# Kernel optimization log

Hardware: AMD Instinct MI355X
Metric: run time of the kernel (lower is better)

The kernel has to match this reference:

```python
import jax, jax.numpy as jnp
import numpy as np

EPS_NUMER = 1e-8   # numerator init in original code
EPS_D2 = 1e-12     # guard sqrt(0) on the (unused) diagonal


def setup_inputs() -> dict:
    key = jax.random.key(0)
    k0, k1, k2, k3 = jax.random.split(key, 4)
    B, T, C, H, W, D, NC = 128, 128, 3, 32, 32, 1024, 10
    data_t = jax.random.normal(k0, (B, T, 1, C, H, W), jnp.float32)
    responses_t = jax.random.normal(k1, (B, T, NC), jnp.float32)
    teaching_signal_t = jax.random.uniform(k2, (B, T, NC), jnp.float32)
    # feature extractor = single linear layer; scaled so distances are moderate
    W_fe = jax.random.normal(k3, (C * H * W, D), jnp.float32) / np.float32(np.sqrt(C * H * W))
    b_fe = jnp.zeros((D,), jnp.float32)
    c = jnp.ones((1,), jnp.float32)
    gamma = jnp.ones((1,), jnp.float32)
    return dict(responses_t=responses_t, data_t=data_t, teaching_signal_t=teaching_signal_t,
                W_fe=W_fe, b_fe=b_fe, c=c, gamma=gamma)


def reference(responses_t, data_t, teaching_signal_t, W_fe, b_fe, c, gamma):
    B, T = data_t.shape[:2]
    # feature extraction: (B*T, C*H*W) @ (C*H*W, D) -> (B, T, 1, D)
    x = data_t.reshape(B * T, -1)
    feats = (x @ W_fe + b_fe).reshape(B, T, 1, -1)
    f = feats[:, :, 0]                                   # (B, T, D)
    # batched pairwise euclidean distance, then extra .sqrt() as in original
    sq = jnp.sum(f * f, axis=-1)                          # (B, T)
    d2 = sq[:, :, None] + sq[:, None, :] - 2.0 * jnp.einsum('bsd,btd->bst', f, f)
    d2 = jnp.maximum(d2, EPS_D2)
    dist = jnp.sqrt(jnp.sqrt(d2))                         # sqrt(cdist) per original
    sims = jnp.exp(-c[0] * dist)                          # (B, S, T)
    # causal weighted sum: numers[b,t,cls] = eps + sum_{s<t} sims[b,s,t]*teach[b,s,cls]
    causal = jnp.tril(jnp.ones((T, T), sims.dtype), -1).T  # mask[s,t] = 1 if s < t
    numers = EPS_NUMER + jnp.einsum('bst,st,bsc->btc', sims, causal, teaching_signal_t)
    tmp = numers ** gamma[0]
    score = tmp / jnp.sum(tmp, axis=-1, keepdims=True)
    # t == 0 uses raw numers (all EPS_NUMER), not normalized
    score = score.at[:, 0].set(EPS_NUMER)
    responses = score[:, :, None, :]                      # (B, T, 1, NC)
    return responses
```

## Files before the change

kernel.cpp:

```cpp
#include <hip/hip_runtime.h>

typedef short short8 __attribute__((ext_vector_type(8)));
typedef float f32x4 __attribute__((ext_vector_type(4)));
typedef int int2v __attribute__((ext_vector_type(2)));
typedef int int4v __attribute__((ext_vector_type(4)));
typedef int int8v __attribute__((ext_vector_type(8)));

#define EPS_NUMER_F 1e-8f
#define EPS_D2_F 1e-12f

#define BB 128
#define TT 128
#define DD 1024
#define CHW 3072
#define NC 10
#define MM (BB * TT)
#define NT 24
#define WSCALE 64.0f
#define INV_WSCALE 0.015625f

#define GLOAD_LDS16(g, l)                                              \
  __builtin_amdgcn_global_load_lds(                                    \
      (const __attribute__((address_space(1))) void*)(g),              \
      (__attribute__((address_space(3))) void*)(l), 16, 0, 0)

#define DS_READ_B128(dst_, off_) \
  asm volatile("ds_read_b128 %0, %1" : "=v"(dst_) : "v"(off_))
#define DS_WRITE_B64(off_, val_) \
  asm volatile("ds_write_b64 %0, %1" :: "v"(off_), "v"(val_))
#define GLB_LOAD_X4(dst_, voff_, imm_) \
  asm volatile("global_load_dwordx4 %0, %1, %2 offset:" #imm_ \
               : "=v"(dst_) : "v"(voff_), "s"(xbase))
#define SCHED_FENCE() __builtin_amdgcn_sched_barrier(0)

#define UNIT_SCALE 0x7f7f7f7f

static __device__ __forceinline__ unsigned lds_addr(const void* p) {
  return (unsigned)(unsigned long long)(const __attribute__((address_space(3))) void*)p;
}

static __device__ __forceinline__ short f2bf(float x) {
  unsigned int u = __float_as_uint(x);
  u = (u + 0x7fffu + ((u >> 16) & 1u)) >> 16;
  return (short)u;
}
static __device__ __forceinline__ float bf2f(short x) {
  return __uint_as_float(((unsigned int)(unsigned short)x) << 16);
}

static __device__ __forceinline__ int2v pk8_fp8(f32x4 a, f32x4 b) {
  int2v r;
  int w0 = __builtin_amdgcn_cvt_pk_fp8_f32(a.x, a.y, 0, false);
  w0 = __builtin_amdgcn_cvt_pk_fp8_f32(a.z, a.w, w0, true);
  int w1 = __builtin_amdgcn_cvt_pk_fp8_f32(b.x, b.y, 0, false);
  w1 = __builtin_amdgcn_cvt_pk_fp8_f32(b.z, b.w, w1, true);
  r.x = w0; r.y = w1;
  return r;
}

__global__ __launch_bounds__(256) void k_transpose_w8(const float* __restrict__ W,
                                                      char* __restrict__ Wt8) {
  __shared__ float tile[32][33];
  const int n0 = blockIdx.x * 32;
  const int k0 = blockIdx.y * 32;
  const int tx = threadIdx.x & 31;
  const int ty = threadIdx.x >> 5;
#pragma unroll
  for (int i = 0; i < 32; i += 8)
    tile[ty + i][tx] = W[(size_t)(k0 + ty + i) * DD + (n0 + tx)];
  __syncthreads();
  const int n = threadIdx.x >> 3;
  const int kq = (threadIdx.x & 7) * 4;
  float a0 = tile[kq + 0][n] * WSCALE;
  float a1 = tile[kq + 1][n] * WSCALE;
  float a2 = tile[kq + 2][n] * WSCALE;
  float a3 = tile[kq + 3][n] * WSCALE;
  int w = __builtin_amdgcn_cvt_pk_fp8_f32(a0, a1, 0, false);
  w = __builtin_amdgcn_cvt_pk_fp8_f32(a2, a3, w, true);
  *reinterpret_cast<int*>(Wt8 + (size_t)(n0 + n) * CHW + (k0 + kq)) = w;
}

__global__ __launch_bounds__(512, 2) void k_gemm_mx(const float* __restrict__ X,
                                                    const char* __restrict__ Wt8,
                                                    const float* __restrict__ bias,
                                                    short* __restrict__ F) {
  __shared__ char As[2][256 * 128];
  __shared__ char Bs[2][256 * 128];

  const int bid = blockIdx.x;
  const int id = (bid & 7) * 32 + (bid >> 3);
  const int bm = (id >> 2) << 8;
  const int bn = (id & 3) << 8;

  const int tid = threadIdx.x;
  const int lane = tid & 63;
  const int wid = tid >> 6;
  const int wr = wid >> 2;
  const int wc = wid & 3;

  const int srow = lane >> 3;
  const int sslot = (lane & 7) ^ (lane >> 3);
  const char* bSrc = Wt8 + (size_t)(bn + srow) * CHW + sslot * 16;

#define STAGE_B_HALF(T_, h_) do {                                            \
    int base_ = (h_) * 128 + wid * 8;                                        \
    GLOAD_LDS16(bSrc + (size_t)(base_) * CHW + (T_) * 128,                   \
                &Bs[(T_) & 1][(base_) * 128]);                               \
    GLOAD_LDS16(bSrc + (size_t)(base_ + 64) * CHW + (T_) * 128,             \
                &Bs[(T_) & 1][(base_ + 64) * 128]);                          \
  } while (0)

  const int arow_st = wid * 16 + (lane >> 3);
  const unsigned long long xbase = (unsigned long long)X;
  unsigned voff[4];
#pragma unroll
  for (int h = 0; h < 2; ++h)
#pragma unroll
    for (int j = 0; j < 2; ++j)
      voff[h * 2 + j] = (unsigned)(((bm + h * 128 + j * 8 + arow_st) * (size_t)CHW
                                    + (lane & 7) * 8) * 4);

  f32x4 ra[8];

#define LOAD_A_KH0() do {                                                    \
    GLB_LOAD_X4(ra[0], voff[0], 0);   GLB_LOAD_X4(ra[1], voff[0], 16);       \
    GLB_LOAD_X4(ra[2], voff[1], 0);   GLB_LOAD_X4(ra[3], voff[1], 16);       \
    GLB_LOAD_X4(ra[4], voff[2], 0);   GLB_LOAD_X4(ra[5], voff[2], 16);       \
    GLB_LOAD_X4(ra[6], voff[3], 0);   GLB_LOAD_X4(ra[7], voff[3], 16);       \
  } while (0)
#define LOAD_A_KH1() do {                                                    \
    GLB_LOAD_X4(ra[0], voff[0], 256); GLB_LOAD_X4(ra[1], voff[0], 272);      \
    GLB_LOAD_X4(ra[2], voff[1], 256); GLB_LOAD_X4(ra[3], voff[1], 272);      \
    GLB_LOAD_X4(ra[4], voff[2], 256); GLB_LOAD_X4(ra[5], voff[2], 272);      \
    GLB_LOAD_X4(ra[6], voff[3], 256); GLB_LOAD_X4(ra[7], voff[3], 272);      \
  } while (0)
#define ADV_A() do { voff[0] += 512; voff[1] += 512; voff[2] += 512; voff[3] += 512; } while (0)

  const int cA = lane & 7;
  const int r8A = lane >> 3;
  unsigned awr0[4], awr1[4];
#pragma unroll
  for (int hj = 0; hj < 4; ++hj) {
    int lrow = (hj >> 1) * 128 + (hj & 1) * 8 + arow_st;
    awr0[hj] = (unsigned)(lrow * 128 + (((cA >> 1)     ^ r8A) * 16) + (cA & 1) * 8);
    awr1[hj] = (unsigned)(lrow * 128 + ((((cA >> 1)+4) ^ r8A) * 16) + (cA & 1) * 8);
  }

#define WRITE_A_KH(T_, kh_) do {                                             \
    unsigned bo_ = (((T_) & 1) ? 32768u : 0u);                               \
    _Pragma("unroll")                                                        \
    for (int hj = 0; hj < 4; ++hj) {                                         \
      int2v w_ = pk8_fp8(ra[hj * 2], ra[hj * 2 + 1]);                        \
      DS_WRITE_B64(aWrBase + ((kh_) ? awr1[hj] : awr0[hj]) + bo_, w_);       \
    }                                                                        \
  } while (0)

  const int fr = lane & 15;
  const int sl = lane >> 4;
  const unsigned fslot0 = (unsigned)((((sl * 2) ^ (fr & 7)) * 16));
  const int arow = wr * 128 + fr;
  const int brow = wc * 64 + fr;

  const unsigned aBase0 = lds_addr(&As[0][0]);
  const unsigned bBase0 = lds_addr(&Bs[0][0]);
  const unsigned aWrBase = aBase0;

  int4v bql[4], bqh[4];
  int4v aql[2], aqh[2];
  f32x4 acc[8][4] = {};

#define READ_B8(bb_) do {                                                    \
    _Pragma("unroll")                                                        \
    for (int ni = 0; ni < 4; ++ni) {                                         \
      unsigned ba_ = (bb_) + (unsigned)((brow + ni * 16) * 128) + fslot0;    \
      DS_READ_B128(bql[ni], ba_);                                            \
      DS_READ_B128(bqh[ni], ba_ ^ 16u);                                      \
    }                                                                        \
  } while (0)
#define READ_A_PAIR(p_, ab_) do {                                            \
    _Pragma("unroll")                                                        \
    for (int m2 = 0; m2 < 2; ++m2) {                                         \
      unsigned aa_ = (ab_) + (unsigned)((arow + (2 * (p_) + m2) * 16) * 128) + fslot0; \
      DS_READ_B128(aql[m2], aa_);                                            \
      DS_READ_B128(aqh[m2], aa_ ^ 16u);                                      \
    }                                                                        \
  } while (0)
#define MFMA8(p_) do {                                                       \
    _Pragma("unroll")                                                        \
    for (int m2 = 0; m2 < 2; ++m2) {                                         \
      int8v av_ = __builtin_shufflevector(aql[m2], aqh[m2], 0,1,2,3,4,5,6,7);\
      _Pragma("unroll")                                                      \
      for (int ni = 0; ni < 4; ++ni) {                                       \
        int8v bv_ = __builtin_shufflevector(bql[ni], bqh[ni], 0,1,2,3,4,5,6,7);\
        acc[2*(p_)+m2][ni] = __builtin_amdgcn_mfma_scale_f32_16x16x128_f8f6f4(\
            av_, bv_, acc[2*(p_)+m2][ni], 0, 0,                              \
            0, UNIT_SCALE, 0, UNIT_SCALE);                                   \
      }                                                                      \
    }                                                                        \
  } while (0)

  LOAD_A_KH0();
  STAGE_B_HALF(0, 0); STAGE_B_HALF(0, 1);
  SCHED_FENCE();
  asm volatile("s_waitcnt vmcnt(4)");
  SCHED_FENCE();
  WRITE_A_KH(0, 0);
  LOAD_A_KH1();
  STAGE_B_HALF(1, 0); STAGE_B_HALF(1, 1);
  SCHED_FENCE();
  asm volatile("s_waitcnt vmcnt(4)");
  SCHED_FENCE();
  WRITE_A_KH(0, 1);
  ADV_A();
  asm volatile("s_waitcnt lgkmcnt(0)");
  SCHED_FENCE();
  __builtin_amdgcn_s_barrier();

  for (int T = 0; T < NT; ++T) {
    const unsigned ab = aBase0 + ((T & 1) ? 32768u : 0u);
    const unsigned bb = bBase0 + ((T & 1) ? 32768u : 0u);

    if (T + 1 < NT) LOAD_A_KH0();
    READ_B8(bb);
    READ_A_PAIR(0, ab);
    SCHED_FENCE();
    __builtin_amdgcn_s_barrier();
    asm volatile("s_waitcnt lgkmcnt(0)");
    SCHED_FENCE();
    __builtin_amdgcn_s_setprio(1);
    MFMA8(0);
    __builtin_amdgcn_s_setprio(0);
    SCHED_FENCE();
    __builtin_amdgcn_s_barrier();

    READ_A_PAIR(1, ab);
    SCHED_FENCE();
    __builtin_amdgcn_s_barrier();
    asm volatile("s_waitcnt lgkmcnt(0)");
    SCHED_FENCE();
    __builtin_amdgcn_s_setprio(1);
    MFMA8(1);
    __builtin_amdgcn_s_setprio(0);
    SCHED_FENCE();
    __builtin_amdgcn_s_barrier();

    READ_A_PAIR(2, ab);
    if (T + 2 < NT) {
      STAGE_B_HALF(T + 2, 0);
      SCHED_FENCE();
      asm volatile("s_waitcnt vmcnt(2)");
      SCHED_FENCE();
    } else if (T + 1 < NT) {
      SCHED_FENCE();
      asm volatile("s_waitcnt vmcnt(0)");
      SCHED_FENCE();
    }
    if (T + 1 < NT) {
      WRITE_A_KH(T + 1, 0);
      LOAD_A_KH1();
    }
    SCHED_FENCE();
    __builtin_amdgcn_s_barrier();
    if (T + 1 < NT) {
      asm volatile("s_waitcnt lgkmcnt(4)");
    } else {
      asm volatile("s_waitcnt lgkmcnt(0)");
    }
    SCHED_FENCE();
    __builtin_amdgcn_s_setprio(1);
    MFMA8(2);
    __builtin_amdgcn_s_setprio(0);
    SCHED_FENCE();
    __builtin_amdgcn_s_barrier();

    READ_A_PAIR(3, ab);
    if (T + 2 < NT) {
      STAGE_B_HALF(T + 2, 1);
      SCHED_FENCE();
      asm volatile("s_waitcnt vmcnt(2)");
      SCHED_FENCE();
    } else if (T + 1 < NT) {
      SCHED_FENCE();
      asm volatile("s_waitcnt vmcnt(0)");
      SCHED_FENCE();
    }
    if (T + 1 < NT) {
      WRITE_A_KH(T + 1, 1);
      ADV_A();
    }
    SCHED_FENCE();
    __builtin_amdgcn_s_barrier();
    if (T + 1 < NT) {
      asm volatile("s_waitcnt lgkmcnt(4)");
    } else {
      asm volatile("s_waitcnt lgkmcnt(0)");
    }
    SCHED_FENCE();
    __builtin_amdgcn_s_setprio(1);
    MFMA8(3);
    __builtin_amdgcn_s_setprio(0);
    asm volatile("s_waitcnt lgkmcnt(0)");
    SCHED_FENCE();
    __builtin_amdgcn_s_barrier();
  }

  const int cc = lane & 15;
  const int crr = sl << 2;
#pragma unroll
  for (int ni = 0; ni < 4; ++ni) {
    int col = bn + wc * 64 + ni * 16 + cc;
    float bv = bias[col];
#pragma unroll
    for (int mi = 0; mi < 8; ++mi) {
      int row0 = bm + wr * 128 + mi * 16 + crr;
#pragma unroll
      for (int q = 0; q < 4; ++q)
        F[(size_t)(row0 + q) * DD + col] = f2bf(acc[mi][ni][q] * INV_WSCALE + bv);
    }
  }
#undef READ_B8
#undef READ_A_PAIR
#undef MFMA8
#undef STAGE_B_HALF
#undef LOAD_A_KH0
#undef LOAD_A_KH1
#undef ADV_A
#undef WRITE_A_KH
}

__global__ __launch_bounds__(256) void k_batch_sims(const short* __restrict__ F,
                                                    const float* __restrict__ teach,
                                                    const float* __restrict__ cptr,
                                                    const float* __restrict__ gptr,
                                                    float* __restrict__ out) {
  __shared__ short ftile[128][40];
  __shared__ float simsT[64][129];
  __shared__ float sqv[128];
  __shared__ float sqp[256];
  __shared__ float teach_s[128][NC];
  __shared__ float numer[64][NC];
  __shared__ float rsum[64];

  const int b = blockIdx.x >> 1;
  const int half = blockIdx.x & 1;
  const int tid = threadIdx.x;
  const int lane = tid & 63;
  const int w = tid >> 6;
  const size_t fbase = (size_t)b * TT * DD;

  for (int idx = tid; idx < TT * NC; idx += 256)
    teach_s[idx / NC][idx % NC] = teach[(size_t)b * TT * NC + idx];

  {
    int row = tid >> 1;
    int kh = (tid & 1) << 9;
    const short* fp = F + fbase + (size_t)row * DD + kh;
    float s = 0.f;
    for (int k = 0; k < 512; k += 8) {
      short8 v = *reinterpret_cast<const short8*>(fp + k);
#pragma unroll
      for (int j = 0; j < 8; ++j) { float x = bf2f(v[j]); s += x * x; }
    }
    sqp[tid] = s;
  }
  __syncthreads();
  if (tid < 128) sqv[tid] = sqp[2 * tid] + sqp[2 * tid + 1];
  __syncthreads();

  f32x4 acc[2][4] = {};
  const int fr = lane & 15;
  const int fk = (lane >> 4) << 3;
  for (int k0 = 0; k0 < DD; k0 += 32) {
#pragma unroll
    for (int i = 0; i < 2; ++i) {
      int idx = tid + (i << 8);
      int row = idx >> 2;
      int kc = (idx & 3) << 3;
      short8 v = *reinterpret_cast<const short8*>(F + fbase + (size_t)row * DD + (k0 + kc));
      *reinterpret_cast<short8*>(&ftile[row][kc]) = v;
    }
    __syncthreads();
    short8 af[2], bfv[4];
#pragma unroll
    for (int mi = 0; mi < 2; ++mi)
      af[mi] = *reinterpret_cast<const short8*>(&ftile[w * 32 + mi * 16 + fr][fk]);
#pragma unroll
    for (int ni = 0; ni < 4; ++ni)
      bfv[ni] = *reinterpret_cast<const short8*>(&ftile[half * 64 + ni * 16 + fr][fk]);
#pragma unroll
    for (int mi = 0; mi < 2; ++mi)
#pragma unroll
      for (int ni = 0; ni < 4; ++ni)
        acc[mi][ni] = __builtin_amdgcn_mfma_f32_16x16x32_bf16(af[mi], bfv[ni], acc[mi][ni], 0, 0, 0);
    __syncthreads();
  }

  const float c0 = cptr[0];
  const int cc = lane & 15;
  const int crr = (lane >> 4) << 2;
#pragma unroll
  for (int mi = 0; mi < 2; ++mi) {
#pragma unroll
    for (int ni = 0; ni < 4; ++ni) {
#pragma unroll
      for (int q = 0; q < 4; ++q) {
        int s_g = w * 32 + mi * 16 + crr + q;
        int tl = ni * 16 + cc;
        int t_g = half * 64 + tl;
        float g = acc[mi][ni][q];
        float d2 = sqv[s_g] + sqv[t_g] - 2.0f * g;
        d2 = fmaxf(d2, EPS_D2_F);
        float dist = sqrtf(sqrtf(d2));
        simsT[tl][s_g] = (s_g < t_g) ? expf(-c0 * dist) : 0.0f;
      }
    }
  }
  __syncthreads();

  const float gam = gptr[0];
  for (int idx = tid; idx < 64 * NC; idx += 256) {
    int tl = idx / NC, c = idx % NC;
    float s = 0.f;
#pragma unroll 4
    for (int si = 0; si < TT; ++si)
      s += simsT[tl][si] * teach_s[si][c];
    float v = EPS_NUMER_F + s;
    numer[tl][c] = (gam == 1.0f) ? v : powf(v, gam);
  }
  __syncthreads();
  if (tid < 64) {
    float s = 0.f;
#pragma unroll
    for (int c = 0; c < NC; ++c) s += numer[tid][c];
    rsum[tid] = s;
  }
  __syncthreads();
  for (int idx = tid; idx < 64 * NC; idx += 256) {
    int tl = idx / NC, c = idx % NC;
    int t_g = half * 64 + tl;
    float v = numer[tl][c] / rsum[tl];
    if (t_g == 0) v = EPS_NUMER_F;
    out[(size_t)b * TT * NC + (size_t)t_g * NC + c] = v;
  }
}

extern "C" void kernel_launch(void* const* d_in, const int* in_sizes, int n_in,
                              void* d_out, int out_size, void* d_ws, size_t ws_size,
                              hipStream_t stream) {
  const float* data = (const float*)d_in[1];
  const float* teach = (const float*)d_in[2];
  const float* Wfe = (const float*)d_in[3];
  const float* bfe = (const float*)d_in[4];
  const float* cp = (const float*)d_in[5];
  const float* gp = (const float*)d_in[6];
  float* outp = (float*)d_out;

  char* ws = (char*)d_ws;
  char* Wt8 = ws;
  short* F = (short*)(ws + (size_t)8 * 1024 * 1024);

  k_transpose_w8<<<dim3(DD / 32, CHW / 32), 256, 0, stream>>>(Wfe, Wt8);
  k_gemm_mx<<<dim3((MM / 256) * (DD / 256)), 512, 0, stream>>>(data, Wt8, bfe, F);
  k_batch_sims<<<dim3(BB * 2), 256, 0, stream>>>(F, teach, cp, gp, outp);
}
```

Baseline: 133.0 us.

## Load GEMM A operand straight from global into MFMA fragments, bypassing LDS

```diff
diff --git a/kernel.cpp b/kernel.cpp
--- a/kernel.cpp
+++ b/kernel.cpp
@@ -26,8 +26,6 @@
 
 #define DS_READ_B128(dst_, off_) \
   asm volatile("ds_read_b128 %0, %1" : "=v"(dst_) : "v"(off_))
-#define DS_WRITE_B64(off_, val_) \
-  asm volatile("ds_write_b64 %0, %1" :: "v"(off_), "v"(val_))
 #define GLB_LOAD_X4(dst_, voff_, imm_) \
   asm volatile("global_load_dwordx4 %0, %1, %2 offset:" #imm_ \
                : "=v"(dst_) : "v"(voff_), "s"(xbase))
@@ -84,7 +82,6 @@
                                                     const char* __restrict__ Wt8,
                                                     const float* __restrict__ bias,
                                                     short* __restrict__ F) {
-  __shared__ char As[2][256 * 128];
   __shared__ char Bs[2][256 * 128];
 
   const int bid = blockIdx.x;
@@ -110,65 +107,33 @@
                 &Bs[(T_) & 1][(base_ + 64) * 128]);                          \
   } while (0)
 
-  const int arow_st = wid * 16 + (lane >> 3);
-  const unsigned long long xbase = (unsigned long long)X;
-  unsigned voff[4];
-#pragma unroll
-  for (int h = 0; h < 2; ++h)
-#pragma unroll
-    for (int j = 0; j < 2; ++j)
-      voff[h * 2 + j] = (unsigned)(((bm + h * 128 + j * 8 + arow_st) * (size_t)CHW
-                                    + (lane & 7) * 8) * 4);
-
-  f32x4 ra[8];
-
-#define LOAD_A_KH0() do {                                                    \
-    GLB_LOAD_X4(ra[0], voff[0], 0);   GLB_LOAD_X4(ra[1], voff[0], 16);       \
-    GLB_LOAD_X4(ra[2], voff[1], 0);   GLB_LOAD_X4(ra[3], voff[1], 16);       \
-    GLB_LOAD_X4(ra[4], voff[2], 0);   GLB_LOAD_X4(ra[5], voff[2], 16);       \
-    GLB_LOAD_X4(ra[6], voff[3], 0);   GLB_LOAD_X4(ra[7], voff[3], 16);       \
-  } while (0)
-#define LOAD_A_KH1() do {                                                    \
-    GLB_LOAD_X4(ra[0], voff[0], 256); GLB_LOAD_X4(ra[1], voff[0], 272);      \
-    GLB_LOAD_X4(ra[2], voff[1], 256); GLB_LOAD_X4(ra[3], voff[1], 272);      \
-    GLB_LOAD_X4(ra[4], voff[2], 256); GLB_LOAD_X4(ra[5], voff[2], 272);      \
-    GLB_LOAD_X4(ra[6], voff[3], 256); GLB_LOAD_X4(ra[7], voff[3], 272);      \
-  } while (0)
-#define ADV_A() do { voff[0] += 512; voff[1] += 512; voff[2] += 512; voff[3] += 512; } while (0)
-
-  const int cA = lane & 7;
-  const int r8A = lane >> 3;
-  unsigned awr0[4], awr1[4];
-#pragma unroll
-  for (int hj = 0; hj < 4; ++hj) {
-    int lrow = (hj >> 1) * 128 + (hj & 1) * 8 + arow_st;
-    awr0[hj] = (unsigned)(lrow * 128 + (((cA >> 1)     ^ r8A) * 16) + (cA & 1) * 8);
-    awr1[hj] = (unsigned)(lrow * 128 + ((((cA >> 1)+4) ^ r8A) * 16) + (cA & 1) * 8);
-  }
-
-#define WRITE_A_KH(T_, kh_) do {                                             \
-    unsigned bo_ = (((T_) & 1) ? 32768u : 0u);                               \
-    _Pragma("unroll")                                                        \
-    for (int hj = 0; hj < 4; ++hj) {                                         \
-      int2v w_ = pk8_fp8(ra[hj * 2], ra[hj * 2 + 1]);                        \
-      DS_WRITE_B64(aWrBase + ((kh_) ? awr1[hj] : awr0[hj]) + bo_, w_);       \
-    }                                                                        \
-  } while (0)
-
   const int fr = lane & 15;
   const int sl = lane >> 4;
   const unsigned fslot0 = (unsigned)((((sl * 2) ^ (fr & 7)) * 16));
-  const int arow = wr * 128 + fr;
   const int brow = wc * 64 + fr;
-
-  const unsigned aBase0 = lds_addr(&As[0][0]);
   const unsigned bBase0 = lds_addr(&Bs[0][0]);
-  const unsigned aWrBase = aBase0;
-
+
+  const unsigned long long xbase = (unsigned long long)X;
+  unsigned voffA[8];
+#pragma unroll
+  for (int m = 0; m < 8; ++m)
+    voffA[m] = (unsigned)((((size_t)(bm + wr * 128 + m * 16 + fr)) * CHW
+                           + sl * 32) * 4);
+
+  f32x4 rx[8];
   int4v bql[4], bqh[4];
-  int4v aql[2], aqh[2];
   f32x4 acc[8][4] = {};
 
+#define LOAD_FRAG(vo_) do {                                                  \
+    GLB_LOAD_X4(rx[0], vo_, 0);   GLB_LOAD_X4(rx[1], vo_, 16);               \
+    GLB_LOAD_X4(rx[2], vo_, 32);  GLB_LOAD_X4(rx[3], vo_, 48);               \
+    GLB_LOAD_X4(rx[4], vo_, 64);  GLB_LOAD_X4(rx[5], vo_, 80);               \
+    GLB_LOAD_X4(rx[6], vo_, 96);  GLB_LOAD_X4(rx[7], vo_, 112);              \
+  } while (0)
+#define ADV_A() do {                                                         \
+    _Pragma("unroll")                                                        \
+    for (int m = 0; m < 8; ++m) voffA[m] += 512u;                            \
+  } while (0)
 #define READ_B8(bb_) do {                                                    \
     _Pragma("unroll")                                                        \
     for (int ni = 0; ni < 4; ++ni) {                                         \
@@ -177,131 +142,91 @@
       DS_READ_B128(bqh[ni], ba_ ^ 16u);                                      \
     }                                                                        \
   } while (0)
-#define READ_A_PAIR(p_, ab_) do {                                            \
+#define CVT_AV(av_) do {                                                     \
+    int2v p0_ = pk8_fp8(rx[0], rx[1]);                                       \
+    int2v p1_ = pk8_fp8(rx[2], rx[3]);                                       \
+    int2v p2_ = pk8_fp8(rx[4], rx[5]);                                       \
+    int2v p3_ = pk8_fp8(rx[6], rx[7]);                                       \
+    av_[0] = p0_.x; av_[1] = p0_.y; av_[2] = p1_.x; av_[3] = p1_.y;          \
+    av_[4] = p2_.x; av_[5] = p2_.y; av_[6] = p3_.x; av_[7] = p3_.y;          \
+  } while (0)
+#define MFMA4(m_, av_) do {                                                  \
     _Pragma("unroll")                                                        \
-    for (int m2 = 0; m2 < 2; ++m2) {                                         \
-      unsigned aa_ = (ab_) + (unsigned)((arow + (2 * (p_) + m2) * 16) * 128) + fslot0; \
-      DS_READ_B128(aql[m2], aa_);                                            \
-      DS_READ_B128(aqh[m2], aa_ ^ 16u);                                      \
+    for (int ni = 0; ni < 4; ++ni) {                                         \
+      int8v bv_ = __builtin_shufflevector(bql[ni], bqh[ni], 0,1,2,3,4,5,6,7);\
+      acc[m_][ni] = __builtin_amdgcn_mfma_scale_f32_16x16x128_f8f6f4(        \
+          av_, bv_, acc[m_][ni], 0, 0, 0, UNIT_SCALE, 0, UNIT_SCALE);        \
     }                                                                        \
   } while (0)
-#define MFMA8(p_) do {                                                       \
-    _Pragma("unroll")                                                        \
-    for (int m2 = 0; m2 < 2; ++m2) {                                         \
-      int8v av_ = __builtin_shufflevector(aql[m2], aqh[m2], 0,1,2,3,4,5,6,7);\
-      _Pragma("unroll")                                                      \
-      for (int ni = 0; ni < 4; ++ni) {                                       \
-        int8v bv_ = __builtin_shufflevector(bql[ni], bqh[ni], 0,1,2,3,4,5,6,7);\
-        acc[2*(p_)+m2][ni] = __builtin_amdgcn_mfma_scale_f32_16x16x128_f8f6f4(\
-            av_, bv_, acc[2*(p_)+m2][ni], 0, 0,                              \
-            0, UNIT_SCALE, 0, UNIT_SCALE);                                   \
-      }                                                                      \
-    }                                                                        \
-  } while (0)
-
-  LOAD_A_KH0();
+
+  LOAD_FRAG(voffA[0]);
   STAGE_B_HALF(0, 0); STAGE_B_HALF(0, 1);
   SCHED_FENCE();
-  asm volatile("s_waitcnt vmcnt(4)");
+  asm volatile("s_waitcnt vmcnt(0)");
   SCHED_FENCE();
-  WRITE_A_KH(0, 0);
-  LOAD_A_KH1();
-  STAGE_B_HALF(1, 0); STAGE_B_HALF(1, 1);
-  SCHED_FENCE();
-  asm volatile("s_waitcnt vmcnt(4)");
-  SCHED_FENCE();
-  WRITE_A_KH(0, 1);
-  ADV_A();
-  asm volatile("s_waitcnt lgkmcnt(0)");
-  SCHED_FENCE();
-  __builtin_amdgcn_s_barrier();
 
   for (int T = 0; T < NT; ++T) {
-    const unsigned ab = aBase0 + ((T & 1) ? 32768u : 0u);
     const unsigned bb = bBase0 + ((T & 1) ? 32768u : 0u);
 
-    if (T + 1 < NT) LOAD_A_KH0();
+    __builtin_amdgcn_s_barrier();
+
     READ_B8(bb);
-    READ_A_PAIR(0, ab);
+    if (T + 1 < NT) {
+      STAGE_B_HALF(T + 1, 0);
+      STAGE_B_HALF(T + 1, 1);
+    }
     SCHED_FENCE();
-    __builtin_amdgcn_s_barrier();
+
+    if (T + 1 < NT) {
+      asm volatile("s_waitcnt vmcnt(4)");
+    } else {
+      asm volatile("s_waitcnt vmcnt(0)");
+    }
+    SCHED_FENCE();
     asm volatile("s_waitcnt lgkmcnt(0)");
     SCHED_FENCE();
-    __builtin_amdgcn_s_setprio(1);
-    MFMA8(0);
-    __builtin_amdgcn_s_setprio(0);
-    SCHED_FENCE();
-    __builtin_amdgcn_s_barrier();
-
-    READ_A_PAIR(1, ab);
-    SCHED_FENCE();
-    __builtin_amdgcn_s_barrier();
-    asm volatile("s_waitcnt lgkmcnt(0)");
-    SCHED_FENCE();
-    __builtin_amdgcn_s_setprio(1);
-    MFMA8(1);
-    __builtin_amdgcn_s_setprio(0);
-    SCHED_FENCE();
-    __builtin_amdgcn_s_barrier();
-
-    READ_A_PAIR(2, ab);
-    if (T + 2 < NT) {
-      STAGE_B_HALF(T + 2, 0);
-      SCHED_FENCE();
-      asm volatile("s_waitcnt vmcnt(2)");
-      SCHED_FENCE();
-    } else if (T + 1 < NT) {
-      SCHED_FENCE();
+    {
+      int8v av;
+      CVT_AV(av);
+      LOAD_FRAG(voffA[1]);
+      SCHED_FENCE();
+      __builtin_amdgcn_s_setprio(1);
+      MFMA4(0, av);
+      __builtin_amdgcn_s_setprio(0);
+      SCHED_FENCE();
+    }
+
+#define ASTEP(m_)                                                            \
+    {                                                                        \
+      asm volatile("s_waitcnt vmcnt(0)");                                    \
+      SCHED_FENCE();                                                         \
+      int8v av;                                                              \
+      CVT_AV(av);                                                            \
+      LOAD_FRAG(voffA[(m_) + 1]);                                            \
+      SCHED_FENCE();                                                         \
+      __builtin_amdgcn_s_setprio(1);                                         \
+      MFMA4(m_, av);                                                         \
+      __builtin_amdgcn_s_setprio(0);                                         \
+      SCHED_FENCE();                                                         \
+    }
+    ASTEP(1) ASTEP(2) ASTEP(3) ASTEP(4) ASTEP(5) ASTEP(6)
+#undef ASTEP
+
+    {
       asm volatile("s_waitcnt vmcnt(0)");
       SCHED_FENCE();
-    }
-    if (T + 1 < NT) {
-      WRITE_A_KH(T + 1, 0);
-      LOAD_A_KH1();
-    }
-    SCHED_FENCE();
-    __builtin_amdgcn_s_barrier();
-    if (T + 1 < NT) {
-      asm volatile("s_waitcnt lgkmcnt(4)");
-    } else {
-      asm volatile("s_waitcnt lgkmcnt(0)");
-    }
-    SCHED_FENCE();
-    __builtin_amdgcn_s_setprio(1);
-    MFMA8(2);
-    __builtin_amdgcn_s_setprio(0);
-    SCHED_FENCE();
-    __builtin_amdgcn_s_barrier();
-
-    READ_A_PAIR(3, ab);
-    if (T + 2 < NT) {
-      STAGE_B_HALF(T + 2, 1);
-      SCHED_FENCE();
-      asm volatile("s_waitcnt vmcnt(2)");
-      SCHED_FENCE();
-    } else if (T + 1 < NT) {
-      SCHED_FENCE();
-      asm volatile("s_waitcnt vmcnt(0)");
-      SCHED_FENCE();
-    }
-    if (T + 1 < NT) {
-      WRITE_A_KH(T + 1, 1);
-      ADV_A();
-    }
-    SCHED_FENCE();
-    __builtin_amdgcn_s_barrier();
-    if (T + 1 < NT) {
-      asm volatile("s_waitcnt lgkmcnt(4)");
-    } else {
-      asm volatile("s_waitcnt lgkmcnt(0)");
-    }
-    SCHED_FENCE();
-    __builtin_amdgcn_s_setprio(1);
-    MFMA8(3);
-    __builtin_amdgcn_s_setprio(0);
-    asm volatile("s_waitcnt lgkmcnt(0)");
-    SCHED_FENCE();
-    __builtin_amdgcn_s_barrier();
+      int8v av;
+      CVT_AV(av);
+      if (T + 1 < NT) {
+        ADV_A();
+        LOAD_FRAG(voffA[0]);
+      }
+      SCHED_FENCE();
+      __builtin_amdgcn_s_setprio(1);
+      MFMA4(7, av);
+      __builtin_amdgcn_s_setprio(0);
+      SCHED_FENCE();
+    }
   }
 
   const int cc = lane & 15;
@@ -319,13 +244,11 @@
     }
   }
 #undef READ_B8
-#undef READ_A_PAIR
-#undef MFMA8
+#undef MFMA4
+#undef CVT_AV
+#undef LOAD_FRAG
+#undef ADV_A
 #undef STAGE_B_HALF
-#undef LOAD_A_KH0
-#undef LOAD_A_KH1
-#undef ADV_A
-#undef WRITE_A_KH
 }
 
 __global__ __launch_bounds__(256) void k_batch_sims(const short* __restrict__ F,
```

Result: slower. 396.5 us (+198.1%).
